# Performance work log

Measured on AMD Instinct MI355X. Metric: run time of the kernel, lower is better.

Reference implementation:

```python
import jax, jax.numpy as jnp
import numpy as np
import math

N = 20000          # nodes
E = 320000         # edges (avg degree 16)
NS, NV = 16, 4     # scalar / vector multiplicities
NCAT = 10
CAT_VOCAB = 119
DIST_DIM = 32
LIG_MAX_R = 5.0
W1_NUMEL = NS * NS + NS * NV          # 320 : layer1 tp weights
W2_NUMEL = NS * NS + NV * NS + NS * NV + NV * NV + NV * NV  # 416


def setup_inputs() -> dict:
    key = jax.random.key(0)
    ks = jax.random.split(key, 24)
    s = 0.1
    inp = {
        'x_cat': jax.random.randint(ks[0], (N, NCAT), 0, 2),
        'x_scalar': jax.random.normal(ks[1], (N, 32), jnp.float32),
        'pos': jax.random.normal(ks[2], (N, 3), jnp.float32) * 3.0,
        'edge_index': jax.random.randint(ks[3], (2, E), 0, N),
        'edge_bond': jax.random.uniform(ks[4], (E, 10), jnp.float32),
        # AtomEncoder params
        'emb_tables': jax.random.normal(ks[5], (NCAT, CAT_VOCAB, NS)) * s,
        'node_w': jax.random.normal(ks[6], (32, NS)) * s,
        'node_b': jnp.zeros((NS,), jnp.float32),
        # lig_edge_embedding MLP (42 -> ns -> ns)
        'em_w1': jax.random.normal(ks[7], (10 + DIST_DIM, NS)) * s,
        'em_b1': jnp.zeros((NS,), jnp.float32),
        'em_w2': jax.random.normal(ks[8], (NS, NS)) * s,
        'em_b2': jnp.zeros((NS,), jnp.float32),
        'c1_w1': jax.random.normal(ks[9], (3 * NS, 3 * NS)) * s,
        'c1_b1': jnp.zeros((3 * NS,), jnp.float32),
        'c1_w2': jax.random.normal(ks[10], (3 * NS, W1_NUMEL)) * s,
        'c1_b2': jnp.zeros((W1_NUMEL,), jnp.float32),
        # conv layer 2 fc
        'c2_w1': jax.random.normal(ks[11], (3 * NS, 3 * NS)) * s,
        'c2_b1': jnp.zeros((3 * NS,), jnp.float32),
        'c2_w2': jax.random.normal(ks[12], (3 * NS, W2_NUMEL)) * s,
        'c2_b2': jnp.zeros((W2_NUMEL,), jnp.float32),
    }
    return inp


def _scatter_mean(vals, idx, n):
    s = jax.ops.segment_sum(vals, idx, num_segments=n)
    cnt = jax.ops.segment_sum(jnp.ones(idx.shape, vals.dtype), idx, num_segments=n)
    return s / jnp.maximum(cnt, 1.0)[:, None]


def _forward(x_cat, x_scalar, pos, edge_index, edge_bond,
             emb_tables, node_w, node_b, em_w1, em_b1, em_w2, em_b2,
             c1_w1, c1_b1, c1_w2, c1_b2, c2_w1, c2_b1, c2_w2, c2_b2):
    ns, nv = NS, NV
    n = x_cat.shape[0]
    # ---- AtomEncoder: sum of categorical embeddings + linear(scalar) ----
    gathered = emb_tables[jnp.arange(NCAT)[None, :], x_cat]      # [N, 10, ns]
    node = gathered.sum(axis=1) + x_scalar @ node_w + node_b    # [N, ns]

    src, dst = edge_index[0], edge_index[1]
    vec = pos[dst] - pos[src]                                   # [E, 3]
    dist = jnp.sqrt(jnp.sum(vec * vec, axis=-1) + 1e-12)
    unit = vec / (dist + 1e-8)[:, None]
    # spherical harmonics, lmax=1, component normalization: [1, sqrt(3)*r_hat]
    sh0 = jnp.ones((vec.shape[0], 1), vec.dtype)
    sh1 = math.sqrt(3.0) * unit                                 # [E, 3]

    # ---- GaussianSmearing + edge embedding MLP ----
    offset = jnp.linspace(0.0, LIG_MAX_R, DIST_DIM)
    coeff = -0.5 / float(LIG_MAX_R / (DIST_DIM - 1)) ** 2
    demb = jnp.exp(coeff * (dist[:, None] - offset[None, :]) ** 2)
    e_in = jnp.concatenate([edge_bond, demb], axis=1)           # [E, 42]
    edge_emb = jax.nn.relu(e_in @ em_w1 + em_b1) @ em_w2 + em_b2  # [E, ns]

    # ======== conv layer 1: ns x0e -> ns x0e + nv x1o ========
    ea = jnp.concatenate([edge_emb, node[src, :ns], node[dst, :ns]], axis=1)
    w = jax.nn.relu(ea @ c1_w1 + c1_b1) @ c1_w2 + c1_b2         # [E, 320]
    wa = w[:, :ns * ns].reshape(-1, ns, ns)
    wb = w[:, ns * ns:].reshape(-1, ns, nv)
    s_dst = node[dst]                                           # [E, ns]
    a = 1.0 / math.sqrt(ns)                                     # fan-in norm
    out0 = jnp.einsum('euk,eu->ek', wa, s_dst) * sh0 * a        # 0e x 0e -> 0e
    out1 = jnp.einsum('euw,eu->ew', wb, s_dst)[:, :, None] * sh1[:, None, :] * a
    tp = jnp.concatenate([out0, out1.reshape(-1, 3 * nv)], axis=1)
    node = _scatter_mean(tp, src, n)                            # [N, ns+3nv]

    # ======== conv layer 2: ns x0e + nv x1o -> ns x0e + nv x1o + nv x1e ====
    ea = jnp.concatenate([edge_emb, node[src, :ns], node[dst, :ns]], axis=1)
    w = jax.nn.relu(ea @ c2_w1 + c2_b1) @ c2_w2 + c2_b2         # [E, 416]
    o = 0
    wa = w[:, o:o + ns * ns].reshape(-1, ns, ns); o += ns * ns
    wb = w[:, o:o + nv * ns].reshape(-1, nv, ns); o += nv * ns
    wc = w[:, o:o + ns * nv].reshape(-1, ns, nv); o += ns * nv
    wd = w[:, o:o + nv * nv].reshape(-1, nv, nv); o += nv * nv
    we = w[:, o:o + nv * nv].reshape(-1, nv, nv)
    s = node[dst, :ns]
    v = node[dst, ns:].reshape(-1, nv, 3)
    a0 = 1.0 / math.sqrt(ns + nv)   # two paths into 0e
    a1 = 1.0 / math.sqrt(ns + nv)   # two paths into 1o
    aE = 1.0 / math.sqrt(nv)        # one path into 1e
    vdot = jnp.einsum('evi,ei->ev', v, sh1)                     # 1o . 1o
    out0 = (jnp.einsum('euk,eu->ek', wa, s) * sh0
            + jnp.einsum('euk,eu->ek', wb, vdot) / math.sqrt(3.0)) * a0
    out1o = (jnp.einsum('euw,eu->ew', wc, s)[:, :, None] * sh1[:, None, :]
             + jnp.einsum('euw,eui->ewi', wd, v) * sh0[:, :, None]) * a1
    crossv = jnp.cross(v, jnp.broadcast_to(sh1[:, None, :], v.shape))
    out1e = jnp.einsum('euw,eui->ewi', we, crossv) * (aE / math.sqrt(2.0))
    tp = jnp.concatenate([out0, out1o.reshape(-1, 3 * nv),
                          out1e.reshape(-1, 3 * nv)], axis=1)
    node = _scatter_mean(tp, src, n)                            # [N, ns+6nv] = [N,40]
    return node


def reference(x_cat, x_scalar, pos, edge_index, edge_bond,
              emb_tables, node_w, node_b, em_w1, em_b1, em_w2, em_b2,
              c1_w1, c1_b1, c1_w2, c1_b2, c2_w1, c2_b1, c2_w2, c2_b2):
    return _forward(x_cat, x_scalar, pos, edge_index, edge_bond,
                    emb_tables, node_w, node_b, em_w1, em_b1, em_w2, em_b2,
                    c1_w1, c1_b1, c1_w2, c1_b2, c2_w1, c2_b1, c2_w2, c2_b2)
```

## Files before the change

### kernel.cpp

```cpp
#include <hip/hip_runtime.h>
#include <math.h>

#define NN 20000
#define NE 320000

typedef _Float16 f16x8 __attribute__((ext_vector_type(8)));
typedef float f32x4 __attribute__((ext_vector_type(4)));
typedef unsigned short ushort_t;
typedef unsigned int uint_t;

#define MFMA16(A,B,C) __builtin_amdgcn_mfma_f32_16x16x32_f16((A),(B),(C),0,0,0)
#define LDS_FENCE() do{ asm volatile("s_waitcnt lgkmcnt(0)" ::: "memory"); __builtin_amdgcn_sched_barrier(0);}while(0)

static_assert(NE % 256 == 0, "edge grid must tile exactly");

__device__ __forceinline__ float frelu(float x){ return fmaxf(x, 0.0f); }

__device__ __forceinline__ void splitf(float x, ushort_t& h, ushort_t& l){
    _Float16 hh = (_Float16)x;
    float r = (x - (float)hh) * 2048.0f;
    _Float16 ll = (_Float16)r;
    union { _Float16 f; ushort_t u; } ch, cl;
    ch.f = hh; cl.f = ll;
    h = ch.u; l = cl.u;
}

__device__ __forceinline__ void edge_embed(
    int e, int s, int d,
    const float* __restrict__ pos,
    const float* __restrict__ edge_bond,
    const float* __restrict__ em_w1, const float* __restrict__ em_b1,
    const float* __restrict__ em_w2, const float* __restrict__ em_b2,
    float* eemb, float* sh1)
{
    float vx = pos[d*3+0] - pos[s*3+0];
    float vy = pos[d*3+1] - pos[s*3+1];
    float vz = pos[d*3+2] - pos[s*3+2];
    float d2 = vx*vx + vy*vy + vz*vz + 1e-12f;
    float dist = sqrtf(d2);
    float inv = 1.0f / (dist + 1e-8f);
    const float SQ3 = 1.7320508075688772f;
    sh1[0] = SQ3 * vx * inv;
    sh1[1] = SQ3 * vy * inv;
    sh1[2] = SQ3 * vz * inv;

    float ein[42];
    #pragma unroll
    for (int t = 0; t < 10; ++t) ein[t] = edge_bond[e*10 + t];
    const float coeff = -19.22f;
    const float step  = 5.0f / 31.0f;
    #pragma unroll
    for (int k = 0; k < 32; ++k) {
        float dd = dist - step * (float)k;
        ein[10+k] = __expf(coeff * dd * dd);
    }

    float t1[16];
    #pragma unroll
    for (int j = 0; j < 16; ++j) t1[j] = em_b1[j];
    #pragma unroll
    for (int t = 0; t < 42; ++t) {
        float v = ein[t];
        #pragma unroll
        for (int j = 0; j < 16; ++j) t1[j] += v * em_w1[t*16 + j];
    }
    #pragma unroll
    for (int j = 0; j < 16; ++j) t1[j] = frelu(t1[j]);

    #pragma unroll
    for (int j = 0; j < 16; ++j) eemb[j] = em_b2[j];
    #pragma unroll
    for (int t = 0; t < 16; ++t) {
        float v = t1[t];
        #pragma unroll
        for (int j = 0; j < 16; ++j) eemb[j] += v * em_w2[t*16 + j];
    }
}

template<int STRIDE>
__device__ __forceinline__ void compute_h(
    int e, int s, int d,
    const float* __restrict__ pos, const float* __restrict__ edge_bond,
    const float* __restrict__ em_w1, const float* __restrict__ em_b1,
    const float* __restrict__ em_w2, const float* __restrict__ em_b2,
    const float* __restrict__ w1, const float* __restrict__ b1,
    const float* __restrict__ node, float* h, float* sh1, float* sdout)
{
    float ea[48];
    edge_embed(e, s, d, pos, edge_bond, em_w1, em_b1, em_w2, em_b2, ea, sh1);
    const float4* rs = reinterpret_cast<const float4*>(node + (size_t)s*STRIDE);
    const float4* rd = reinterpret_cast<const float4*>(node + (size_t)d*STRIDE);
    #pragma unroll
    for (int k = 0; k < 4; ++k) {
        float4 q = rs[k];
        ea[16+4*k] = q.x; ea[17+4*k] = q.y; ea[18+4*k] = q.z; ea[19+4*k] = q.w;
        float4 r = rd[k];
        ea[32+4*k] = r.x; ea[33+4*k] = r.y; ea[34+4*k] = r.z; ea[35+4*k] = r.w;
    }
    #pragma unroll
    for (int k = 0; k < 16; ++k) sdout[k] = ea[32+k];
    #pragma unroll
    for (int j = 0; j < 48; ++j) h[j] = b1[j];
    #pragma unroll
    for (int t = 0; t < 48; ++t) {
        float v = ea[t];
        #pragma unroll
        for (int j = 0; j < 48; ++j) h[j] += v * w1[t*48 + j];
    }
    #pragma unroll
    for (int j = 0; j < 48; ++j) h[j] = frelu(h[j]);
}

__global__ __launch_bounds__(256)
void k_pack(const float* __restrict__ w2, const float* __restrict__ b2,
            ushort_t* __restrict__ out, int NC, int ntiles)
{
    int slot = blockIdx.x*256 + threadIdx.x;
    if (slot >= ntiles*128) return;
    int tl = slot >> 7; int r7 = slot & 127; int kb = r7 >> 6; int ll = r7 & 63;
    int col = tl*16 + (ll & 15);
    int k0 = (kb<<5) + ((ll>>4)<<3);
    uint_t hw[4], lw[4];
    #pragma unroll
    for (int p = 0; p < 4; ++p) {
        int ka = k0 + 2*p, kb2 = k0 + 2*p + 1;
        float va = (ka < 48) ? w2[ka*NC + col] : (ka == 48 ? b2[col] : 0.0f);
        float vb = (kb2 < 48) ? w2[kb2*NC + col] : (kb2 == 48 ? b2[col] : 0.0f);
        ushort_t ah, al, bh, bl;
        splitf(va, ah, al);
        splitf(vb, bh, bl);
        hw[p] = (uint_t)ah | ((uint_t)bh << 16);
        lw[p] = (uint_t)al | ((uint_t)bl << 16);
    }
    int base = tl*2048 + kb*1024 + ll*8;
    *reinterpret_cast<uint4*>(&out[base])       = make_uint4(hw[0], hw[1], hw[2], hw[3]);
    *reinterpret_cast<uint4*>(&out[base + 512]) = make_uint4(lw[0], lw[1], lw[2], lw[3]);
}

struct B4 { f16x8 h0, l0, h1, l1; };
__device__ __forceinline__ B4 loadB(const f16x8* __restrict__ g, int t, int l) {
    B4 b;
    const f16x8* p = g + t*256 + l;
    b.h0 = p[0];
    b.l0 = p[64];
    b.h1 = p[128];
    b.l1 = p[192];
    return b;
}

__device__ __forceinline__ void stage_A(ushort_t* bounce, int l,
                                        const uint_t* hph, const uint_t* hpl,
                                        f16x8 ahi[4][2], f16x8 alo[4][2])
{
    #pragma unroll
    for (int t = 0; t < 4; ++t)
        *reinterpret_cast<uint4*>(&bounce[l*32 + t*8]) = make_uint4(0,0,0,0);
    LDS_FENCE();
    #pragma unroll
    for (int mt = 0; mt < 4; ++mt) {
        if ((l >> 4) == mt) {
            #pragma unroll
            for (int jj = 0; jj < 25; ++jj) {
                int k = jj*2, kb = k >> 5, kk = k & 31;
                int lr = (l & 15) + ((kk >> 3) << 4);
                int off = kb*512 + lr*8 + (kk & 7);
                *reinterpret_cast<uint_t*>(&bounce[off])        = hph[jj];
                *reinterpret_cast<uint_t*>(&bounce[1024 + off]) = hpl[jj];
            }
        }
        LDS_FENCE();
        ahi[mt][0] = *reinterpret_cast<const f16x8*>(&bounce[l*8]);
        ahi[mt][1] = *reinterpret_cast<const f16x8*>(&bounce[512 + l*8]);
        alo[mt][0] = *reinterpret_cast<const f16x8*>(&bounce[1024 + l*8]);
        alo[mt][1] = *reinterpret_cast<const f16x8*>(&bounce[1536 + l*8]);
        LDS_FENCE();
    }
}

__global__ __launch_bounds__(256)
void k_node_feat(const int* __restrict__ x_cat, const float* __restrict__ x_scalar,
                 const float* __restrict__ emb, const float* __restrict__ node_w,
                 const float* __restrict__ node_b, float* __restrict__ node0)
{
    int n = blockIdx.x * 256 + threadIdx.x;
    if (n >= NN) return;
    float acc[16];
    #pragma unroll
    for (int k = 0; k < 16; ++k) acc[k] = node_b[k];
    #pragma unroll
    for (int c = 0; c < 10; ++c) {
        int idx = x_cat[n*10 + c];
        const float4* row = reinterpret_cast<const float4*>(emb + (c*119 + idx)*16);
        #pragma unroll
        for (int k = 0; k < 4; ++k) {
            float4 q = row[k];
            acc[4*k+0] += q.x; acc[4*k+1] += q.y; acc[4*k+2] += q.z; acc[4*k+3] += q.w;
        }
    }
    #pragma unroll
    for (int t = 0; t < 32; ++t) {
        float xs = x_scalar[n*32 + t];
        #pragma unroll
        for (int k = 0; k < 16; ++k) acc[k] += xs * node_w[t*16 + k];
    }
    #pragma unroll
    for (int k = 0; k < 16; ++k) node0[n*16 + k] = acc[k];
}

__global__ __launch_bounds__(256)
void k_edge_l1(const int* __restrict__ ei, const float* __restrict__ pos,
               const float* __restrict__ edge_bond,
               const float* __restrict__ em_w1, const float* __restrict__ em_b1,
               const float* __restrict__ em_w2, const float* __restrict__ em_b2,
               const float* __restrict__ w1, const float* __restrict__ b1,
               const ushort_t* __restrict__ packW,
               const float* __restrict__ node0,
               float* __restrict__ accum, float* __restrict__ cnt)
{
    __shared__ __align__(16) unsigned char smem[20736];
    float* sT  = (float*)smem;
    float* sSh = (float*)(smem + 16640);
    int*   sSrc= (int*)(smem + 19712);

    int tid = threadIdx.x;
    int l = tid & 63;
    int cc = l & 15;
    int e = blockIdx.x*256 + tid;
    int s = ei[e], d = ei[NE + e];

    float h[48], sh1[3], sd[16];
    compute_h<16>(e, s, d, pos, edge_bond, em_w1, em_b1, em_w2, em_b2, w1, b1,
                  node0, h, sh1, sd);
    atomicAdd(cnt + s, 1.0f);

    uint_t hph[25], hpl[25];
    #pragma unroll
    for (int jj = 0; jj < 24; ++jj) {
        ushort_t ah, al, bh, bl;
        splitf(h[2*jj],   ah, al);
        splitf(h[2*jj+1], bh, bl);
        hph[jj] = (uint_t)ah | ((uint_t)bh << 16);
        hpl[jj] = (uint_t)al | ((uint_t)bl << 16);
    }
    hph[24] = 0x3C00u;
    hpl[24] = 0u;

    f16x8 ahi[4][2], alo[4][2];
    stage_A((ushort_t*)smem + (tid >> 6)*2048, l, hph, hpl, ahi, alo);

    __syncthreads();
    sSrc[tid] = s;
    #pragma unroll
    for (int u = 0; u < 16; ++u) sT[u*260 + tid] = sd[u];
    #pragma unroll
    for (int k = 0; k < 3; ++k) sSh[tid*3 + k] = sh1[k];
    __syncthreads();

    f32x4 out0[4];
    float ob[4][4];
    #pragma unroll
    for (int mt = 0; mt < 4; ++mt) {
        out0[mt] = (f32x4){0.f,0.f,0.f,0.f};
        #pragma unroll
        for (int r = 0; r < 4; ++r) ob[mt][r] = 0.f;
    }

    const f16x8* gB = reinterpret_cast<const f16x8*>(packW);
    B4 cur = loadB(gB, 0, l);
    #pragma unroll 1
    for (int t = 0; t < 20; ++t) {
        B4 nxt;
        if (t + 1 < 20) nxt = loadB(gB, t + 1, l);
        #pragma unroll
        for (int mt = 0; mt < 4; ++mt) {
            f32x4 Dh = (f32x4){0.f,0.f,0.f,0.f};
            f32x4 Dc = (f32x4){0.f,0.f,0.f,0.f};
            Dh = MFMA16(ahi[mt][0], cur.h0, Dh);
            Dh = MFMA16(ahi[mt][1], cur.h1, Dh);
            Dc = MFMA16(alo[mt][0], cur.h0, Dc);
            Dc = MFMA16(ahi[mt][0], cur.l0, Dc);
            Dc = MFMA16(alo[mt][1], cur.h1, Dc);
            Dc = MFMA16(ahi[mt][1], cur.l1, Dc);
            f32x4 D = Dh + Dc * 0.00048828125f;
            int elb = (tid & 192) + (mt << 4) + ((l >> 4) << 2);
            if (t < 16) {
                f32x4 sv = *reinterpret_cast<const f32x4*>(&sT[t*260 + elb]);
                out0[mt] += sv * D;
            } else {
                const float* sp = &sT[(((t-16)<<2) + (cc>>2))*260 + elb];
                #pragma unroll
                for (int r = 0; r < 4; ++r) ob[mt][r] += sp[r] * D[r];
            }
        }
        cur = nxt;
    }

    #pragma unroll
    for (int mt = 0; mt < 4; ++mt) {
        int elb = (tid & 192) + (mt << 4) + ((l >> 4) << 2);
        #pragma unroll
        for (int r = 0; r < 4; ++r) {
            int el = elb + r;
            int sidx = sSrc[el];
            atomicAdd(accum + (size_t)sidx*28 + cc, out0[mt][r] * 0.25f);
            float x = ob[mt][r];
            x += __shfl_xor(x, 4); x += __shfl_xor(x, 8);
            int q = cc / 3; int i = cc - q*3;
            float xq = __shfl(x, (l & 48) | q);
            if (cc < 12)
                atomicAdd(accum + (size_t)sidx*28 + 16 + cc, 0.25f * xq * sSh[el*3 + i]);
        }
    }
}

__global__ __launch_bounds__(256)
void k_edge_l2(const int* __restrict__ ei, const float* __restrict__ pos,
               const float* __restrict__ edge_bond,
               const float* __restrict__ em_w1, const float* __restrict__ em_b1,
               const float* __restrict__ em_w2, const float* __restrict__ em_b2,
               const float* __restrict__ w1, const float* __restrict__ b1,
               const ushort_t* __restrict__ packW,
               const float* __restrict__ node1,
               float* __restrict__ accum2)
{
    __shared__ __align__(16) unsigned char smem[25920];
    float* sT  = (float*)smem;
    float* sVd = (float*)(smem + 16640);
    float* sSh = (float*)(smem + 20800);
    int*   sSrc= (int*)(smem + 23872);
    int*   sDst= (int*)(smem + 24896);

    int tid = threadIdx.x;
    int l = tid & 63;
    int cc = l & 15;
    int e = blockIdx.x*256 + tid;
    int s = ei[e], d = ei[NE + e];

    float h[48], sh1[3], sd[16];
    compute_h<28>(e, s, d, pos, edge_bond, em_w1, em_b1, em_w2, em_b2, w1, b1,
                  node1, h, sh1, sd);

    float vdr[4];
    {
        const float4* rv = reinterpret_cast<const float4*>(node1 + (size_t)d*28 + 16);
        float4 a = rv[0], b = rv[1], c = rv[2];
        float vv[12] = {a.x,a.y,a.z,a.w, b.x,b.y,b.z,b.w, c.x,c.y,c.z,c.w};
        const float INV_SQ3 = 0.5773502691896258f;
        #pragma unroll
        for (int u = 0; u < 4; ++u)
            vdr[u] = (vv[u*3]*sh1[0] + vv[u*3+1]*sh1[1] + vv[u*3+2]*sh1[2]) * INV_SQ3;
    }

    uint_t hph[25], hpl[25];
    #pragma unroll
    for (int jj = 0; jj < 24; ++jj) {
        ushort_t ah, al, bh, bl;
        splitf(h[2*jj],   ah, al);
        splitf(h[2*jj+1], bh, bl);
        hph[jj] = (uint_t)ah | ((uint_t)bh << 16);
        hpl[jj] = (uint_t)al | ((uint_t)bl << 16);
    }
    hph[24] = 0x3C00u;
    hpl[24] = 0u;

    f16x8 ahi[4][2], alo[4][2];
    stage_A((ushort_t*)smem + (tid >> 6)*2048, l, hph, hpl, ahi, alo);

    __syncthreads();
    sSrc[tid] = s;
    sDst[tid] = d;
    #pragma unroll
    for (int u = 0; u < 16; ++u) sT[u*260 + tid] = sd[u];
    #pragma unroll
    for (int u = 0; u < 4; ++u) sVd[u*260 + tid] = vdr[u];
    #pragma unroll
    for (int k = 0; k < 3; ++k) sSh[tid*3 + k] = sh1[k];
    __syncthreads();

    const float A0 = 0.22360679774997896f;
    const float AE = 0.3535533905932738f;

    f32x4 out0[4];
    float outc[4][4];
    #pragma unroll
    for (int mt = 0; mt < 4; ++mt) {
        out0[mt] = (f32x4){0.f,0.f,0.f,0.f};
        #pragma unroll
        for (int r = 0; r < 4; ++r) outc[mt][r] = 0.f;
    }

    const f16x8* gB = reinterpret_cast<const f16x8*>(packW);
    B4 cur = loadB(gB, 0, l);
    #pragma unroll 1
    for (int t = 0; t < 26; ++t) {
        B4 nxt;
        if (t + 1 < 26) nxt = loadB(gB, t + 1, l);
        #pragma unroll
        for (int mt = 0; mt < 4; ++mt) {
            f32x4 Dh = (f32x4){0.f,0.f,0.f,0.f};
            f32x4 Dc = (f32x4){0.f,0.f,0.f,0.f};
            Dh = MFMA16(ahi[mt][0], cur.h0, Dh);
            Dh = MFMA16(ahi[mt][1], cur.h1, Dh);
            Dc = MFMA16(alo[mt][0], cur.h0, Dc);
            Dc = MFMA16(ahi[mt][0], cur.l0, Dc);
            Dc = MFMA16(alo[mt][1], cur.h1, Dc);
            Dc = MFMA16(ahi[mt][1], cur.l1, Dc);
            f32x4 D = Dh + Dc * 0.00048828125f;
            int elb = (tid & 192) + (mt << 4) + ((l >> 4) << 2);
            if (t < 16) {
                f32x4 sv = *reinterpret_cast<const f32x4*>(&sT[t*260 + elb]);
                out0[mt] += sv * D;
            } else if (t < 20) {
                f32x4 vd = *reinterpret_cast<const f32x4*>(&sVd[(t-16)*260 + elb]);
                out0[mt] += vd * D;
            } else if (t < 24) {
                const float* sp = &sT[(((t-20)<<2) + (cc>>2))*260 + elb];
                #pragma unroll
                for (int r = 0; r < 4; ++r) outc[mt][r] += sp[r] * D[r];
            } else if (t == 24) {
                #pragma unroll
                for (int r = 0; r < 4; ++r) {
                    int el = elb + r;
                    int dv = sDst[el];
                    const float* vp = node1 + (size_t)dv*28 + 16 + (cc>>2)*3;
                    float a0 = D[r]*vp[0], a1 = D[r]*vp[1], a2 = D[r]*vp[2];
                    a0 += __shfl_xor(a0,4); a0 += __shfl_xor(a0,8);
                    a1 += __shfl_xor(a1,4); a1 += __shfl_xor(a1,8);
                    a2 += __shfl_xor(a2,4); a2 += __shfl_xor(a2,8);
                    float xc = outc[mt][r];
                    xc += __shfl_xor(xc,4); xc += __shfl_xor(xc,8);
                    int q = cc / 3; int i = cc - q*3;
                    int srcl = (l & 48) | q;
                    float g0 = __shfl(a0, srcl), g1 = __shfl(a1, srcl), g2 = __shfl(a2, srcl);
                    float oo = (i==0) ? g0 : ((i==1) ? g1 : g2);
                    float xq = __shfl(xc, srcl);
                    if (cc < 12) {
                        float sh1i = sSh[el*3 + i];
                        atomicAdd(accum2 + (size_t)sSrc[el]*40 + 16 + cc,
                                  A0 * (xq * sh1i + oo));
                    }
                }
            } else {
                #pragma unroll
                for (int r = 0; r < 4; ++r) {
                    int el = elb + r;
                    int dv = sDst[el];
                    const float* vp = node1 + (size_t)dv*28 + 16 + (cc>>2)*3;
                    float vx = vp[0], vy = vp[1], vz = vp[2];
                    float sx = sSh[el*3+0], sy = sSh[el*3+1], sz = sSh[el*3+2];
                    float cx = vy*sz - vz*sy;
                    float cy = vz*sx - vx*sz;
                    float cz = vx*sy - vy*sx;
                    float a0 = D[r]*cx, a1 = D[r]*cy, a2 = D[r]*cz;
                    a0 += __shfl_xor(a0,4); a0 += __shfl_xor(a0,8);
                    a1 += __shfl_xor(a1,4); a1 += __shfl_xor(a1,8);
                    a2 += __shfl_xor(a2,4); a2 += __shfl_xor(a2,8);
                    int q = cc / 3; int i = cc - q*3;
                    int srcl = (l & 48) | q;
                    float g0 = __shfl(a0, srcl), g1 = __shfl(a1, srcl), g2 = __shfl(a2, srcl);
                    float oo = (i==0) ? g0 : ((i==1) ? g1 : g2);
                    if (cc < 12)
                        atomicAdd(accum2 + (size_t)sSrc[el]*40 + 28 + cc, AE * oo);
                }
            }
        }
        cur = nxt;
    }

    #pragma unroll
    for (int mt = 0; mt < 4; ++mt) {
        int elb = (tid & 192) + (mt << 4) + ((l >> 4) << 2);
        #pragma unroll
        for (int r = 0; r < 4; ++r) {
            int el = elb + r;
            atomicAdd(accum2 + (size_t)sSrc[el]*40 + cc, out0[mt][r] * A0);
        }
    }
}

__global__ __launch_bounds__(256)
void k_div(const float* in, float* out, const float* __restrict__ cnt, int cols, int total)
{
    int i = blockIdx.x * 256 + threadIdx.x;
    if (i >= total) return;
    int n = i / cols;
    out[i] = in[i] / fmaxf(cnt[n], 1.0f);
}

extern "C" void kernel_launch(void* const* d_in, const int* in_sizes, int n_in,
                              void* d_out, int out_size, void* d_ws, size_t ws_size,
                              hipStream_t stream) {
    const int*   x_cat     = (const int*)  d_in[0];
    const float* x_scalar  = (const float*)d_in[1];
    const float* pos       = (const float*)d_in[2];
    const int*   ei        = (const int*)  d_in[3];
    const float* edge_bond = (const float*)d_in[4];
    const float* emb       = (const float*)d_in[5];
    const float* node_w    = (const float*)d_in[6];
    const float* node_b    = (const float*)d_in[7];
    const float* em_w1     = (const float*)d_in[8];
    const float* em_b1     = (const float*)d_in[9];
    const float* em_w2     = (const float*)d_in[10];
    const float* em_b2     = (const float*)d_in[11];
    const float* c1_w1     = (const float*)d_in[12];
    const float* c1_b1     = (const float*)d_in[13];
    const float* c1_w2     = (const float*)d_in[14];
    const float* c1_b2     = (const float*)d_in[15];
    const float* c2_w1     = (const float*)d_in[16];
    const float* c2_b1     = (const float*)d_in[17];
    const float* c2_w2     = (const float*)d_in[18];
    const float* c2_b2     = (const float*)d_in[19];

    float* ws     = (float*)d_ws;
    float* node0  = ws;
    float* accum1 = ws + 320000;
    float* accum2 = ws + 880000;
    float* cnt    = ws + 1680000;
    ushort_t* packA = (ushort_t*)(ws + 1700000);
    ushort_t* packB = packA + 20*2048;

    hipMemsetAsync(accum1, 0, (size_t)(560000 + 800000 + 20000) * sizeof(float), stream);

    k_pack<<<(20*128 + 255) / 256, 256, 0, stream>>>(c1_w2, c1_b2, packA, 320, 20);
    k_pack<<<(26*128 + 255) / 256, 256, 0, stream>>>(c2_w2, c2_b2, packB, 416, 26);

    k_node_feat<<<(NN + 255) / 256, 256, 0, stream>>>(
        x_cat, x_scalar, emb, node_w, node_b, node0);

    k_edge_l1<<<NE / 256, 256, 0, stream>>>(
        ei, pos, edge_bond, em_w1, em_b1, em_w2, em_b2,
        c1_w1, c1_b1, packA, node0, accum1, cnt);

    k_div<<<(560000 + 255) / 256, 256, 0, stream>>>(accum1, accum1, cnt, 28, 560000);

    k_edge_l2<<<NE / 256, 256, 0, stream>>>(
        ei, pos, edge_bond, em_w1, em_b1, em_w2, em_b2,
        c2_w1, c2_b1, packB, accum1, accum2);

    k_div<<<(800000 + 255) / 256, 256, 0, stream>>>(accum2, (float*)d_out, cnt, 40, 800000);
}
```

Baseline: 328.6 us.

## Precompute edge embeddings and per-node first-layer projections, reuse across both conv layers

Edge embedding and spherical harmonics are computed once in a new pre-pass and stored to global memory, so both edge layers read them instead of recomputing the 42->16->16 MLP. The src/dst node parts of the first fc layer (48x48) are factored into per-node projections computed once per node (20000 nodes) rather than per edge (320000 edges). Layer 2 also stages destination vector features in LDS instead of re-gathering them from global memory, and the B-tile loads are double-prefetched two steps ahead. The cost is extra global traffic (about 20 MB of edge embeddings plus the node projections), additional kernel launches, and larger LDS use in layer 2, which may lower occupancy.

```diff
diff --git a/kernel.cpp b/kernel.cpp
--- a/kernel.cpp
+++ b/kernel.cpp
@@ -77,38 +77,63 @@
     }
 }
 
-template<int STRIDE>
-__device__ __forceinline__ void compute_h(
-    int e, int s, int d,
-    const float* __restrict__ pos, const float* __restrict__ edge_bond,
-    const float* __restrict__ em_w1, const float* __restrict__ em_b1,
-    const float* __restrict__ em_w2, const float* __restrict__ em_b2,
-    const float* __restrict__ w1, const float* __restrict__ b1,
-    const float* __restrict__ node, float* h, float* sh1, float* sdout)
-{
-    float ea[48];
-    edge_embed(e, s, d, pos, edge_bond, em_w1, em_b1, em_w2, em_b2, ea, sh1);
-    const float4* rs = reinterpret_cast<const float4*>(node + (size_t)s*STRIDE);
-    const float4* rd = reinterpret_cast<const float4*>(node + (size_t)d*STRIDE);
+__global__ __launch_bounds__(256)
+void k_edge_pre(const int* __restrict__ ei, const float* __restrict__ pos,
+                const float* __restrict__ edge_bond,
+                const float* __restrict__ em_w1, const float* __restrict__ em_b1,
+                const float* __restrict__ em_w2, const float* __restrict__ em_b2,
+                float* __restrict__ eembG, float* __restrict__ eshG,
+                float* __restrict__ cnt)
+{
+    int e = blockIdx.x*256 + threadIdx.x;
+    int s = ei[e], d = ei[NE + e];
+    float em[16], sh1[3];
+    edge_embed(e, s, d, pos, edge_bond, em_w1, em_b1, em_w2, em_b2, em, sh1);
+    float4* pe = reinterpret_cast<float4*>(eembG + (size_t)e*16);
+    #pragma unroll
+    for (int k = 0; k < 4; ++k)
+        pe[k] = make_float4(em[4*k], em[4*k+1], em[4*k+2], em[4*k+3]);
+    reinterpret_cast<float4*>(eshG)[e] = make_float4(sh1[0], sh1[1], sh1[2], 0.f);
+    atomicAdd(cnt + s, 1.0f);
+}
+
+__global__ __launch_bounds__(256)
+void k_node_y(const float* __restrict__ node, int stride,
+              const float* __restrict__ w1, float* __restrict__ y)
+{
+    int n = blockIdx.x*256 + threadIdx.x;
+    if (n >= NN) return;
+    float sv[16];
+    const float4* r = reinterpret_cast<const float4*>(node + (size_t)n*stride);
     #pragma unroll
     for (int k = 0; k < 4; ++k) {
-        float4 q = rs[k];
-        ea[16+4*k] = q.x; ea[17+4*k] = q.y; ea[18+4*k] = q.z; ea[19+4*k] = q.w;
-        float4 r = rd[k];
-        ea[32+4*k] = r.x; ea[33+4*k] = r.y; ea[34+4*k] = r.z; ea[35+4*k] = r.w;
-    }
-    #pragma unroll
-    for (int k = 0; k < 16; ++k) sdout[k] = ea[32+k];
-    #pragma unroll
-    for (int j = 0; j < 48; ++j) h[j] = b1[j];
-    #pragma unroll
-    for (int t = 0; t < 48; ++t) {
-        float v = ea[t];
-        #pragma unroll
-        for (int j = 0; j < 48; ++j) h[j] += v * w1[t*48 + j];
-    }
-    #pragma unroll
-    for (int j = 0; j < 48; ++j) h[j] = frelu(h[j]);
+        float4 q = r[k];
+        sv[4*k]=q.x; sv[4*k+1]=q.y; sv[4*k+2]=q.z; sv[4*k+3]=q.w;
+    }
+    float yb[48];
+    #pragma unroll
+    for (int j = 0; j < 48; ++j) yb[j] = 0.f;
+    #pragma unroll
+    for (int t = 0; t < 16; ++t) {
+        float v = sv[t];
+        #pragma unroll
+        for (int j = 0; j < 48; ++j) yb[j] += v * w1[(16+t)*48 + j];
+    }
+    float* yo = y + (size_t)n*96;
+    #pragma unroll
+    for (int j = 0; j < 12; ++j)
+        reinterpret_cast<float4*>(yo)[j] = make_float4(yb[4*j], yb[4*j+1], yb[4*j+2], yb[4*j+3]);
+    #pragma unroll
+    for (int j = 0; j < 48; ++j) yb[j] = 0.f;
+    #pragma unroll
+    for (int t = 0; t < 16; ++t) {
+        float v = sv[t];
+        #pragma unroll
+        for (int j = 0; j < 48; ++j) yb[j] += v * w1[(32+t)*48 + j];
+    }
+    #pragma unroll
+    for (int j = 0; j < 12; ++j)
+        reinterpret_cast<float4*>(yo + 48)[j] = make_float4(yb[4*j], yb[4*j+1], yb[4*j+2], yb[4*j+3]);
 }
 
 __global__ __launch_bounds__(256)
@@ -177,6 +202,40 @@
     }
 }
 
+__device__ __forceinline__ void build_h(
+    int e, int s, int d,
+    const float* __restrict__ eembG,
+    const float* __restrict__ y,
+    const float* __restrict__ w1, const float* __restrict__ b1,
+    float* h)
+{
+    float em[16];
+    const float4* pe = reinterpret_cast<const float4*>(eembG + (size_t)e*16);
+    #pragma unroll
+    for (int k = 0; k < 4; ++k) {
+        float4 q = pe[k];
+        em[4*k]=q.x; em[4*k+1]=q.y; em[4*k+2]=q.z; em[4*k+3]=q.w;
+    }
+    #pragma unroll
+    for (int j = 0; j < 48; ++j) h[j] = b1[j];
+    #pragma unroll
+    for (int t = 0; t < 16; ++t) {
+        float v = em[t];
+        #pragma unroll
+        for (int j = 0; j < 48; ++j) h[j] += v * w1[t*48 + j];
+    }
+    const float4* pb = reinterpret_cast<const float4*>(y + (size_t)s*96);
+    const float4* pc = reinterpret_cast<const float4*>(y + (size_t)d*96 + 48);
+    #pragma unroll
+    for (int kk = 0; kk < 12; ++kk) {
+        float4 qb = pb[kk], qc = pc[kk];
+        h[4*kk+0] = frelu(h[4*kk+0] + qb.x + qc.x);
+        h[4*kk+1] = frelu(h[4*kk+1] + qb.y + qc.y);
+        h[4*kk+2] = frelu(h[4*kk+2] + qb.z + qc.z);
+        h[4*kk+3] = frelu(h[4*kk+3] + qb.w + qc.w);
+    }
+}
+
 __global__ __launch_bounds__(256)
 void k_node_feat(const int* __restrict__ x_cat, const float* __restrict__ x_scalar,
                  const float* __restrict__ emb, const float* __restrict__ node_w,
@@ -208,14 +267,13 @@
 }
 
 __global__ __launch_bounds__(256)
-void k_edge_l1(const int* __restrict__ ei, const float* __restrict__ pos,
-               const float* __restrict__ edge_bond,
-               const float* __restrict__ em_w1, const float* __restrict__ em_b1,
-               const float* __restrict__ em_w2, const float* __restrict__ em_b2,
+void k_edge_l1(const int* __restrict__ ei,
                const float* __restrict__ w1, const float* __restrict__ b1,
                const ushort_t* __restrict__ packW,
+               const float* __restrict__ eembG, const float* __restrict__ eshG,
+               const float* __restrict__ y,
                const float* __restrict__ node0,
-               float* __restrict__ accum, float* __restrict__ cnt)
+               float* __restrict__ accum)
 {
     __shared__ __align__(16) unsigned char smem[20736];
     float* sT  = (float*)smem;
@@ -228,10 +286,18 @@
     int e = blockIdx.x*256 + tid;
     int s = ei[e], d = ei[NE + e];
 
-    float h[48], sh1[3], sd[16];
-    compute_h<16>(e, s, d, pos, edge_bond, em_w1, em_b1, em_w2, em_b2, w1, b1,
-                  node0, h, sh1, sd);
-    atomicAdd(cnt + s, 1.0f);
+    float4 shv = reinterpret_cast<const float4*>(eshG)[e];
+    float sd[16];
+    {
+        const float4* rd = reinterpret_cast<const float4*>(node0 + (size_t)d*16);
+        #pragma unroll
+        for (int k = 0; k < 4; ++k) {
+            float4 q = rd[k];
+            sd[4*k]=q.x; sd[4*k+1]=q.y; sd[4*k+2]=q.z; sd[4*k+3]=q.w;
+        }
+    }
+    float h[48];
+    build_h(e, s, d, eembG, y, w1, b1, h);
 
     uint_t hph[25], hpl[25];
     #pragma unroll
@@ -252,8 +318,7 @@
     sSrc[tid] = s;
     #pragma unroll
     for (int u = 0; u < 16; ++u) sT[u*260 + tid] = sd[u];
-    #pragma unroll
-    for (int k = 0; k < 3; ++k) sSh[tid*3 + k] = sh1[k];
+    sSh[tid*3+0] = shv.x; sSh[tid*3+1] = shv.y; sSh[tid*3+2] = shv.z;
     __syncthreads();
 
     f32x4 out0[4];
@@ -266,11 +331,8 @@
     }
 
     const f16x8* gB = reinterpret_cast<const f16x8*>(packW);
-    B4 cur = loadB(gB, 0, l);
-    #pragma unroll 1
-    for (int t = 0; t < 20; ++t) {
-        B4 nxt;
-        if (t + 1 < 20) nxt = loadB(gB, t + 1, l);
+
+    auto process = [&](int t, const B4& cur) {
         #pragma unroll
         for (int mt = 0; mt < 4; ++mt) {
             f32x4 Dh = (f32x4){0.f,0.f,0.f,0.f};
@@ -292,7 +354,16 @@
                 for (int r = 0; r < 4; ++r) ob[mt][r] += sp[r] * D[r];
             }
         }
-        cur = nxt;
+    };
+
+    B4 b0 = loadB(gB, 0, l), b1v = loadB(gB, 1, l);
+    #pragma unroll 1
+    for (int t = 0; t < 20; t += 2) {
+        B4 p0 = (t + 2 < 20) ? loadB(gB, t + 2, l) : b0;
+        process(t, b0);
+        B4 p1 = (t + 3 < 20) ? loadB(gB, t + 3, l) : b1v;
+        process(t + 1, b1v);
+        b0 = p0; b1v = p1;
     }
 
     #pragma unroll
@@ -314,21 +385,20 @@
 }
 
 __global__ __launch_bounds__(256)
-void k_edge_l2(const int* __restrict__ ei, const float* __restrict__ pos,
-               const float* __restrict__ edge_bond,
-               const float* __restrict__ em_w1, const float* __restrict__ em_b1,
-               const float* __restrict__ em_w2, const float* __restrict__ em_b2,
+void k_edge_l2(const int* __restrict__ ei,
                const float* __restrict__ w1, const float* __restrict__ b1,
                const ushort_t* __restrict__ packW,
+               const float* __restrict__ eembG, const float* __restrict__ eshG,
+               const float* __restrict__ y,
                const float* __restrict__ node1,
                float* __restrict__ accum2)
 {
-    __shared__ __align__(16) unsigned char smem[25920];
+    __shared__ __align__(16) unsigned char smem[37376];
     float* sT  = (float*)smem;
     float* sVd = (float*)(smem + 16640);
-    float* sSh = (float*)(smem + 20800);
-    int*   sSrc= (int*)(smem + 23872);
-    int*   sDst= (int*)(smem + 24896);
+    float* sV  = (float*)(smem + 20800);
+    float* sSh = (float*)(smem + 33280);
+    int*   sSrc= (int*)(smem + 36352);
 
     int tid = threadIdx.x;
     int l = tid & 63;
@@ -336,20 +406,30 @@
     int e = blockIdx.x*256 + tid;
     int s = ei[e], d = ei[NE + e];
 
-    float h[48], sh1[3], sd[16];
-    compute_h<28>(e, s, d, pos, edge_bond, em_w1, em_b1, em_w2, em_b2, w1, b1,
-                  node1, h, sh1, sd);
-
+    float4 shv = reinterpret_cast<const float4*>(eshG)[e];
+    float sh1[3] = {shv.x, shv.y, shv.z};
+    float sd[16], vv[12];
+    {
+        const float4* rd = reinterpret_cast<const float4*>(node1 + (size_t)d*28);
+        #pragma unroll
+        for (int k = 0; k < 4; ++k) {
+            float4 q = rd[k];
+            sd[4*k]=q.x; sd[4*k+1]=q.y; sd[4*k+2]=q.z; sd[4*k+3]=q.w;
+        }
+        #pragma unroll
+        for (int k = 0; k < 3; ++k) {
+            float4 q = rd[4+k];
+            vv[4*k]=q.x; vv[4*k+1]=q.y; vv[4*k+2]=q.z; vv[4*k+3]=q.w;
+        }
+    }
     float vdr[4];
-    {
-        const float4* rv = reinterpret_cast<const float4*>(node1 + (size_t)d*28 + 16);
-        float4 a = rv[0], b = rv[1], c = rv[2];
-        float vv[12] = {a.x,a.y,a.z,a.w, b.x,b.y,b.z,b.w, c.x,c.y,c.z,c.w};
-        const float INV_SQ3 = 0.5773502691896258f;
-        #pragma unroll
-        for (int u = 0; u < 4; ++u)
-            vdr[u] = (vv[u*3]*sh1[0] + vv[u*3+1]*sh1[1] + vv[u*3+2]*sh1[2]) * INV_SQ3;
-    }
+    const float INV_SQ3 = 0.5773502691896258f;
+    #pragma unroll
+    for (int u = 0; u < 4; ++u)
+        vdr[u] = (vv[u*3]*sh1[0] + vv[u*3+1]*sh1[1] + vv[u*3+2]*sh1[2]) * INV_SQ3;
+
+    float h[48];
+    build_h(e, s, d, eembG, y, w1, b1, h);
 
     uint_t hph[25], hpl[25];
     #pragma unroll
@@ -368,13 +448,13 @@
 
     __syncthreads();
     sSrc[tid] = s;
-    sDst[tid] = d;
     #pragma unroll
     for (int u = 0; u < 16; ++u) sT[u*260 + tid] = sd[u];
     #pragma unroll
     for (int u = 0; u < 4; ++u) sVd[u*260 + tid] = vdr[u];
     #pragma unroll
-    for (int k = 0; k < 3; ++k) sSh[tid*3 + k] = sh1[k];
+    for (int k = 0; k < 12; ++k) sV[k*260 + tid] = vv[k];
+    sSh[tid*3+0] = shv.x; sSh[tid*3+1] = shv.y; sSh[tid*3+2] = shv.z;
     __syncthreads();
 
     const float A0 = 0.22360679774997896f;
@@ -390,11 +470,8 @@
     }
 
     const f16x8* gB = reinterpret_cast<const f16x8*>(packW);
-    B4 cur = loadB(gB, 0, l);
-    #pragma unroll 1
-    for (int t = 0; t < 26; ++t) {
-        B4 nxt;
-        if (t + 1 < 26) nxt = loadB(gB, t + 1, l);
+
+    auto process = [&](int t, const B4& cur) {
         #pragma unroll
         for (int mt = 0; mt < 4; ++mt) {
             f32x4 Dh = (f32x4){0.f,0.f,0.f,0.f};
@@ -418,12 +495,14 @@
                 #pragma unroll
                 for (int r = 0; r < 4; ++r) outc[mt][r] += sp[r] * D[r];
             } else if (t == 24) {
+                int base3 = (cc >> 2) * 3;
                 #pragma unroll
                 for (int r = 0; r < 4; ++r) {
                     int el = elb + r;
-                    int dv = sDst[el];
-                    const float* vp = node1 + (size_t)dv*28 + 16 + (cc>>2)*3;
-                    float a0 = D[r]*vp[0], a1 = D[r]*vp[1], a2 = D[r]*vp[2];
+                    float vx = sV[(base3+0)*260 + el];
+                    float vy = sV[(base3+1)*260 + el];
+                    float vz = sV[(base3+2)*260 + el];
+                    float a0 = D[r]*vx, a1 = D[r]*vy, a2 = D[r]*vz;
                     a0 += __shfl_xor(a0,4); a0 += __shfl_xor(a0,8);
                     a1 += __shfl_xor(a1,4); a1 += __shfl_xor(a1,8);
                     a2 += __shfl_xor(a2,4); a2 += __shfl_xor(a2,8);
@@ -441,12 +520,13 @@
                     }
                 }
             } else {
+                int base3 = (cc >> 2) * 3;
                 #pragma unroll
                 for (int r = 0; r < 4; ++r) {
                     int el = elb + r;
-                    int dv = sDst[el];
-                    const float* vp = node1 + (size_t)dv*28 + 16 + (cc>>2)*3;
-                    float vx = vp[0], vy = vp[1], vz = vp[2];
+                    float vx = sV[(base3+0)*260 + el];
+                    float vy = sV[(base3+1)*260 + el];
+                    float vz = sV[(base3+2)*260 + el];
                     float sx = sSh[el*3+0], sy = sSh[el*3+1], sz = sSh[el*3+2];
                     float cx = vy*sz - vz*sy;
                     float cy = vz*sx - vx*sz;
@@ -464,7 +544,16 @@
                 }
             }
         }
-        cur = nxt;
+    };
+
+    B4 b0 = loadB(gB, 0, l), b1v = loadB(gB, 1, l);
+    #pragma unroll 1
+    for (int t = 0; t < 26; t += 2) {
+        B4 p0 = (t + 2 < 26) ? loadB(gB, t + 2, l) : b0;
+        process(t, b0);
+        B4 p1 = (t + 3 < 26) ? loadB(gB, t + 3, l) : b1v;
+        process(t + 1, b1v);
+        b0 = p0; b1v = p1;
     }
 
     #pragma unroll
@@ -518,6 +607,9 @@
     float* cnt    = ws + 1680000;
     ushort_t* packA = (ushort_t*)(ws + 1700000);
     ushort_t* packB = packA + 20*2048;
+    float* eembG  = ws + 1747104;
+    float* eshG   = ws + 6867104;
+    float* yBuf   = ws + 8147104;
 
     hipMemsetAsync(accum1, 0, (size_t)(560000 + 800000 + 20000) * sizeof(float), stream);
 
@@ -527,15 +619,20 @@
     k_node_feat<<<(NN + 255) / 256, 256, 0, stream>>>(
         x_cat, x_scalar, emb, node_w, node_b, node0);
 
+    k_edge_pre<<<NE / 256, 256, 0, stream>>>(
+        ei, pos, edge_bond, em_w1, em_b1, em_w2, em_b2, eembG, eshG, cnt);
+
+    k_node_y<<<(NN + 255) / 256, 256, 0, stream>>>(node0, 16, c1_w1, yBuf);
+
     k_edge_l1<<<NE / 256, 256, 0, stream>>>(
-        ei, pos, edge_bond, em_w1, em_b1, em_w2, em_b2,
-        c1_w1, c1_b1, packA, node0, accum1, cnt);
+        ei, c1_w1, c1_b1, packA, eembG, eshG, yBuf, node0, accum1);
 
     k_div<<<(560000 + 255) / 256, 256, 0, stream>>>(accum1, accum1, cnt, 28, 560000);
 
+    k_node_y<<<(NN + 255) / 256, 256, 0, stream>>>(accum1, 28, c2_w1, yBuf);
+
     k_edge_l2<<<NE / 256, 256, 0, stream>>>(
-        ei, pos, edge_bond, em_w1, em_b1, em_w2, em_b2,
-        c2_w1, c2_b1, packB, accum1, accum2);
+        ei, c2_w1, c2_b1, packB, eembG, eshG, yBuf, accum1, accum2);
 
     k_div<<<(800000 + 255) / 256, 256, 0, stream>>>(accum2, (float*)d_out, cnt, 40, 800000);
 }
```

Result: slower. 345.1 us (+5.0%).
